# Performance work log

Hardware: AMD Instinct MI355X
Metric: run time of the kernel (lower is better)

The kernel has to match this reference:

```python
import math
import jax, jax.numpy as jnp
import numpy as np

HEADS = 8
DIM_HEAD = 64
NUM_MEM_KV = 16


def alibi_slopes(heads):
    def pow2_slopes(n):
        start = 2 ** (-(2 ** -(math.log2(n) - 3)))
        return [start * (start ** i) for i in range(n)]
    if math.log2(heads).is_integer():
        return np.asarray(pow2_slopes(heads), dtype=np.float32)
    cp2 = 2 ** math.floor(math.log2(heads))
    extra = pow2_slopes(2 * cp2)[0::2][: heads - cp2]
    return np.asarray(pow2_slopes(cp2) + extra, dtype=np.float32)


def setup_inputs() -> dict:
    key = jax.random.key(0)
    ks = jax.random.split(key, 12)
    b, n, dim = 2, 2048, 512
    h, dh, mem = HEADS, DIM_HEAD, NUM_MEM_KV
    s = 0.02  # weight init scale for numerical sanity
    return {
        "x": jax.random.normal(ks[0], (b, n, dim), jnp.float32),
        "Wq": jax.random.normal(ks[1], (dim, h * dh), jnp.float32) * s,
        "Wk": jax.random.normal(ks[2], (dim, h * dh), jnp.float32) * s,
        "Wv": jax.random.normal(ks[3], (dim, h * dh), jnp.float32) * s,
        "mem_k": jax.random.normal(ks[4], (h, mem, dh), jnp.float32),
        "mem_v": jax.random.normal(ks[5], (h, mem, dh), jnp.float32),
        "pre_proj": jax.random.normal(ks[6], (h, h), jnp.float32),
        "post_proj": jax.random.normal(ks[7], (h, h), jnp.float32),
        "head_scale_params": jnp.ones((1, h, 1, 1), jnp.float32),
        "Wout": jax.random.normal(ks[8], (h * dh, dim), jnp.float32) * s,
        "bout": jnp.zeros((dim,), jnp.float32),
    }


def reference(x, Wq, Wk, Wv, mem_k, mem_v, pre_proj, post_proj,
              head_scale_params, Wout, bout):
    b, n, dim = x.shape
    h, dh, mem = HEADS, DIM_HEAD, NUM_MEM_KV
    scale = dh ** -0.5

    def split_heads(t):  # [b,n,h*dh] -> [b,h,n,dh]
        return t.reshape(b, n, h, dh).transpose(0, 2, 1, 3)

    q = split_heads(x @ Wq)
    k = split_heads(x @ Wk)
    v = split_heads(x @ Wv)

    # prepend learned memory key/values: k,v -> [b,h,mem+n,dh]
    k = jnp.concatenate([jnp.broadcast_to(mem_k, (b, h, mem, dh)), k], axis=2)
    v = jnp.concatenate([jnp.broadcast_to(mem_v, (b, h, mem, dh)), v], axis=2)
    j = mem + n

    dots = jnp.einsum('bhid,bhjd->bhij', q, k) * scale
    # talking heads (pre-softmax)
    dots = jnp.einsum('bhij,hk->bkij', dots, pre_proj)
    # alibi relative positional bias: arange(j) * slope per head
    slopes = jnp.asarray(alibi_slopes(h))  # [h]
    dots = dots + jnp.arange(j, dtype=dots.dtype)[None, None, None, :] * slopes[None, :, None, None]
    # causal mask (mem columns always visible); mask where col-mem > row
    neg = -jnp.finfo(dots.dtype).max
    causal = (jnp.arange(j)[None, :] - mem) > jnp.arange(n)[:, None]  # [n,j]
    dots = jnp.where(causal[None, None], neg, dots)

    attn = jax.nn.softmax(dots, axis=-1)
    # talking heads (post-softmax)
    attn = jnp.einsum('bhij,hk->bkij', attn, post_proj)

    out = jnp.einsum('bhij,bhjd->bhid', attn, v)
    out = out * head_scale_params
    out = out.transpose(0, 2, 1, 3).reshape(b, n, h * dh)
    return out @ Wout + bout
```

## Files before the change

### kernel.cpp

```cpp
#include <hip/hip_runtime.h>
#include <math.h>

namespace {
constexpr int B = 2;
constexpr int N = 2048;
constexpr int DIM = 512;
constexpr int H = 8;
constexpr int MEM = 16;
constexpr int J = MEM + N;
constexpr int CHUNK = 256;
constexpr int CMAX = 9;
constexpr float S2 = 0.125f * 1.4426950408889634f;
constexpr size_t EPB = 17170432;
}

typedef __attribute__((ext_vector_type(8))) short short8;
typedef __attribute__((ext_vector_type(4))) float floatx4;
typedef __attribute__((ext_vector_type(4))) unsigned short ushortx4;
typedef __attribute__((ext_vector_type(8))) unsigned short ushortx8;

__device__ inline unsigned short f2bf(float f) {
    unsigned int u = __float_as_uint(f);
    u += 0x7fffu + ((u >> 16) & 1u);
    return (unsigned short)(u >> 16);
}
__device__ inline unsigned int pk2bf(float a, float b) {
    return ((__float_as_uint(a) + 0x8000u) >> 16) |
           ((__float_as_uint(b) + 0x8000u) & 0xffff0000u);
}

__global__ __launch_bounds__(256)
void wt_conv(const float* __restrict__ Wq, const float* __restrict__ Wk,
             const float* __restrict__ Wv, const float* __restrict__ Wo,
             unsigned short* __restrict__ tq, unsigned short* __restrict__ tk,
             unsigned short* __restrict__ tv, unsigned short* __restrict__ to_)
{
    const int z = blockIdx.z;
    const float* __restrict__ W = (z == 0) ? Wq : (z == 1) ? Wk : (z == 2) ? Wv : Wo;
    unsigned short* __restrict__ WT = (z == 0) ? tq : (z == 1) ? tk : (z == 2) ? tv : to_;
    const int k0 = blockIdx.x * 64, n0 = blockIdx.y * 64;

    __shared__ __align__(16) unsigned short tile[64][72];
    const int t = threadIdx.x;
    const int rrow = t >> 4, rcol = (t & 15) * 4;
#pragma unroll
    for (int rr = 0; rr < 4; ++rr) {
        const int row = rrow + rr * 16;
        const float4 v = *(const float4*)(W + (size_t)(k0 + row) * DIM + n0 + rcol);
        tile[rcol + 0][row] = f2bf(v.x);
        tile[rcol + 1][row] = f2bf(v.y);
        tile[rcol + 2][row] = f2bf(v.z);
        tile[rcol + 3][row] = f2bf(v.w);
    }
    __syncthreads();
    const int orow = t >> 2, oseg = (t & 3) * 16;
    *(ushortx8*)(WT + (size_t)(n0 + orow) * DIM + k0 + oseg) =
        *(const ushortx8*)(&tile[orow][oseg]);
    *(ushortx8*)(WT + (size_t)(n0 + orow) * DIM + k0 + oseg + 8) =
        *(const ushortx8*)(&tile[orow][oseg + 8]);
}

__global__ __launch_bounds__(256)
void qkv_gemm(const float* __restrict__ x, const unsigned short* __restrict__ tq,
              const unsigned short* __restrict__ tk, const unsigned short* __restrict__ tv,
              unsigned short* __restrict__ q16, unsigned short* __restrict__ k16,
              unsigned short* __restrict__ vt16)
{
    const int which = blockIdx.z;
    const unsigned short* __restrict__ WT = (which == 0) ? tq : (which == 1) ? tk : tv;
    const int t = threadIdx.x;
    const int lane = t & 63, w = t >> 6;
    const int iL = lane & 15, quad = lane >> 4;
    const int mb = blockIdx.x * 64;
    const int n0 = blockIdx.y * 64;

    __shared__ __align__(16) unsigned short As[2][64][32];
    __shared__ __align__(16) unsigned short Bs[2][64][32];

    const int ar0 = t >> 3, as4 = (t & 7) * 4;
    const int br0 = t >> 2, bs8 = (t & 3) * 8;

    floatx4 acc[4];
#pragma unroll
    for (int ng = 0; ng < 4; ++ng) acc[ng] = (floatx4){0.f, 0.f, 0.f, 0.f};

    {
        const float4 v0 = *(const float4*)(x + (size_t)(mb + ar0) * DIM + as4);
        const float4 v1 = *(const float4*)(x + (size_t)(mb + ar0 + 32) * DIM + as4);
        ushortx4 o0 = { f2bf(v0.x), f2bf(v0.y), f2bf(v0.z), f2bf(v0.w) };
        ushortx4 o1 = { f2bf(v1.x), f2bf(v1.y), f2bf(v1.z), f2bf(v1.w) };
        *(ushortx4*)(&As[0][ar0][as4]) = o0;
        *(ushortx4*)(&As[0][ar0 + 32][as4]) = o1;
        *(ushortx8*)(&Bs[0][br0][bs8]) =
            *(const ushortx8*)(WT + (size_t)(n0 + br0) * DIM + bs8);
    }
    __syncthreads();

#pragma unroll
    for (int it = 0; it < 16; ++it) {
        const int buf = it & 1;
        if (it + 1 < 16) {
            const int k0 = (it + 1) * 32;
            const float4 v0 = *(const float4*)(x + (size_t)(mb + ar0) * DIM + k0 + as4);
            const float4 v1 = *(const float4*)(x + (size_t)(mb + ar0 + 32) * DIM + k0 + as4);
            const ushortx8 bv =
                *(const ushortx8*)(WT + (size_t)(n0 + br0) * DIM + k0 + bs8);
            ushortx4 o0 = { f2bf(v0.x), f2bf(v0.y), f2bf(v0.z), f2bf(v0.w) };
            ushortx4 o1 = { f2bf(v1.x), f2bf(v1.y), f2bf(v1.z), f2bf(v1.w) };
            *(ushortx4*)(&As[buf ^ 1][ar0][as4]) = o0;
            *(ushortx4*)(&As[buf ^ 1][ar0 + 32][as4]) = o1;
            *(ushortx8*)(&Bs[buf ^ 1][br0][bs8]) = bv;
        }
        const short8 af = *(const short8*)(&As[buf][w * 16 + iL][quad * 8]);
#pragma unroll
        for (int ng = 0; ng < 4; ++ng) {
            const short8 bf = *(const short8*)(&Bs[buf][ng * 16 + iL][quad * 8]);
            acc[ng] = __builtin_amdgcn_mfma_f32_16x16x32_bf16(af, bf, acc[ng], 0, 0, 0);
        }
        __syncthreads();
    }

    const int mbw = mb + w * 16;
    const int h0 = n0 >> 6;
    if (which == 2) {
#pragma unroll
        for (int ng = 0; ng < 4; ++ng) {
            const int d = ng * 16 + iL;
#pragma unroll
            for (int r = 0; r < 4; ++r) {
                const int m = mbw + quad * 4 + r;
                const int bb = m >> 11, ii = m & (N - 1);
                vt16[((size_t)(bb * H + h0) * 64 + d) * J + MEM + ii] = f2bf(acc[ng][r]);
            }
        }
    } else {
        unsigned short* dst = (which == 0) ? q16 : k16;
#pragma unroll
        for (int ng = 0; ng < 4; ++ng) {
            const int d = ng * 16 + iL;
#pragma unroll
            for (int r = 0; r < 4; ++r) {
                const int m = mbw + quad * 4 + r;
                const int bb = m >> 11, ii = m & (N - 1);
                const size_t rowbase = (which == 0)
                    ? ((size_t)(bb * H + h0) * N + ii)
                    : ((size_t)(bb * H + h0) * J + MEM + ii);
                dst[rowbase * 64 + d] = f2bf(acc[ng][r]);
            }
        }
    }
}

__global__ void memkv_copy(const float* __restrict__ mem_k, const float* __restrict__ mem_v,
                           unsigned short* __restrict__ k16, unsigned short* __restrict__ vt16)
{
    const int idx = blockIdx.x * 256 + threadIdx.x;
    if (idx >= H * MEM * 64) return;
    const int h0 = idx >> 10;
    const int rd = idx & 1023;
    const int r = rd >> 6, d = rd & 63;
    const unsigned short kk = f2bf(mem_k[idx]);
    const unsigned short vv = f2bf(mem_v[idx]);
#pragma unroll
    for (int bb = 0; bb < B; ++bb) {
        k16[((size_t)(bb * H + h0) * J + r) * 64 + d] = kk;
        vt16[((size_t)(bb * H + h0) * 64 + d) * J + r] = vv;
    }
}

__global__ __launch_bounds__(256)
void attn_scores(const unsigned short* __restrict__ qb, const unsigned short* __restrict__ kb,
                 const float* __restrict__ prep, float* __restrict__ lbuf,
                 unsigned short* __restrict__ e16)
{
    const int c = blockIdx.x, tt = 127 - blockIdx.y, b = blockIdx.z;
    const int i0 = tt * 16;
    const int jlim = i0 + 32;
    const int jstart = c * CHUNK;
    if (jstart >= jlim) return;
    const int jend = min(jstart + CHUNK, jlim);

    __shared__ __align__(16) unsigned short q_s[8][16][64];
    __shared__ __align__(16) float pre_s[64];
    const int t = threadIdx.x;
    if (t < 64) pre_s[t] = prep[t];
#pragma unroll
    for (int u4 = 0; u4 < 4; ++u4) {
        const int u = t + u4 * 256;
        const int h = u >> 7, rem = u & 127, i = rem >> 3, seg = (rem & 7) * 8;
        *(ushortx8*)(&q_s[h][i][seg]) =
            *(const ushortx8*)(qb + ((size_t)(b * H + h) * N + i0 + i) * 64 + seg);
    }
    __syncthreads();

    const int lane = t & 63, w = t >> 6;
    const int iL = lane & 15, quad = lane >> 4;
    const int i = i0 + iL;
    const size_t ebase = (size_t)b * EPB + (size_t)(8 * tt * tt + 24 * tt) * 128;

    float l_acc[8];
#pragma unroll
    for (int h1 = 0; h1 < 8; ++h1) l_acc[h1] = 0.f;

    bool any = false;
    for (int j0 = jstart + w * 16; j0 < jend; j0 += 64) {
        any = true;
        float dots[8][4];
#pragma unroll
        for (int h1 = 0; h1 < 8; ++h1)
#pragma unroll
            for (int r = 0; r < 4; ++r) dots[h1][r] = 0.f;

        const unsigned short* kp0 = kb + ((size_t)(b * H) * J + j0 + iL) * 64 + quad * 8;
        short8 kc0 = *(const short8*)kp0;
        short8 kc1 = *(const short8*)(kp0 + 32);
#pragma unroll
        for (int h0 = 0; h0 < 8; ++h0) {
            short8 kn0, kn1;
            if (h0 < 7) {
                const unsigned short* kpn =
                    kb + ((size_t)(b * H + h0 + 1) * J + j0 + iL) * 64 + quad * 8;
                kn0 = *(const short8*)kpn;
                kn1 = *(const short8*)(kpn + 32);
            }
            const short8 qf0 = *(const short8*)(&q_s[h0][iL][quad * 8]);
            const short8 qf1 = *(const short8*)(&q_s[h0][iL][quad * 8 + 32]);
            floatx4 a = {0.f, 0.f, 0.f, 0.f};
            a = __builtin_amdgcn_mfma_f32_16x16x32_bf16(kc0, qf0, a, 0, 0, 0);
            a = __builtin_amdgcn_mfma_f32_16x16x32_bf16(kc1, qf1, a, 0, 0, 0);
            const float4 pr0 = *(const float4*)(&pre_s[h0 * 8]);
            const float4 pr1 = *(const float4*)(&pre_s[h0 * 8 + 4]);
#pragma unroll
            for (int r = 0; r < 4; ++r) {
                const float av = a[r];
                dots[0][r] = fmaf(av, pr0.x, dots[0][r]);
                dots[1][r] = fmaf(av, pr0.y, dots[1][r]);
                dots[2][r] = fmaf(av, pr0.z, dots[2][r]);
                dots[3][r] = fmaf(av, pr0.w, dots[3][r]);
                dots[4][r] = fmaf(av, pr1.x, dots[4][r]);
                dots[5][r] = fmaf(av, pr1.y, dots[5][r]);
                dots[6][r] = fmaf(av, pr1.z, dots[6][r]);
                dots[7][r] = fmaf(av, pr1.w, dots[7][r]);
            }
            kc0 = kn0; kc1 = kn1;
        }

        unsigned int epk[4][4];
        float etmp[4];
#pragma unroll
        for (int h1 = 0; h1 < 8; ++h1) {
            const float slopeE = 1.4426950408889634f / (float)(2 << h1);
#pragma unroll
            for (int r = 0; r < 4; ++r) {
                const int j = j0 + quad * 4 + r;
                const bool vis = (j - MEM) <= i;
                const float e = vis ? exp2f(fmaf(dots[h1][r], S2, slopeE * (float)(j - i - MEM)))
                                    : 0.f;
                l_acc[h1] += e;
                if (h1 & 1) epk[r][h1 >> 1] = pk2bf(etmp[r], e);
                else        etmp[r] = e;
            }
        }
#pragma unroll
        for (int r = 0; r < 4; ++r) {
            uint4 o = make_uint4(epk[r][0], epk[r][1], epk[r][2], epk[r][3]);
            *(uint4*)(e16 + ebase + (size_t)((j0 + quad * 4 + r) * 16 + iL) * 8) = o;
        }
    }

#pragma unroll
    for (int h1 = 0; h1 < 8; ++h1) {
        float v = l_acc[h1];
        v += __shfl_xor(v, 16);
        v += __shfl_xor(v, 32);
        if (quad == 0 && any)
            atomicAdd(lbuf + ((size_t)(b * 128 + tt) * 8 + h1) * 16 + iL, v);
    }
}

__global__ __launch_bounds__(256)
void attn_pv2(const unsigned short* __restrict__ e16, const unsigned short* __restrict__ vt,
              const float* __restrict__ postp, const float* __restrict__ hsp,
              const float* __restrict__ lbuf, float* __restrict__ ao)
{
    const int c = blockIdx.x, tt = 127 - blockIdx.y, b = blockIdx.z;
    const int i0 = tt * 16;
    const int jlim = i0 + 32;
    const int jstart = c * CHUNK;
    if (jstart >= jlim) return;
    const int jend = min(jstart + CHUNK, jlim);
    const int nw = (jend - jstart + 31) >> 5;

    __shared__ __align__(16) unsigned short p2s[2][8][16][40];
    __shared__ __align__(16) float post_s[64];

    const int t = threadIdx.x;
    if (t < 64) post_s[t] = postp[t] * hsp[t & 7];

    const int lane = t & 63, w = t >> 6;
    const int iL = lane & 15, quad = lane >> 4;
    const int dW = w * 16 + iL;
    const int i_p = t & 15;
    const int jj = t >> 4;
    const size_t ebase = (size_t)b * EPB + (size_t)(8 * tt * tt + 24 * tt) * 128;

    float linv[8];
#pragma unroll
    for (int h1 = 0; h1 < 8; ++h1)
        linv[h1] = 1.0f / lbuf[((size_t)(b * 128 + tt) * 8 + h1) * 16 + i_p];

    floatx4 y[8];
#pragma unroll
    for (int h2 = 0; h2 < 8; ++h2) y[h2] = (floatx4){0.f, 0.f, 0.f, 0.f};

    ushortx8 evc[2], evn[2];
    {
        const int j0c = jstart + jj * 2;
        const int ja = min(j0c, jend - 1), jb2 = min(j0c + 1, jend - 1);
        evc[0] = *(const ushortx8*)(e16 + ebase + (size_t)(ja * 16 + i_p) * 8);
        evc[1] = *(const ushortx8*)(e16 + ebase + (size_t)(jb2 * 16 + i_p) * 8);
    }
    __syncthreads();

    for (int n = 0; n < nw; ++n) {
        const int jw0 = jstart + n * 32;
        {
            const int j0n = jstart + (n + 1) * 32 + jj * 2;
            const int ja = min(j0n, jend - 1), jb2 = min(j0n + 1, jend - 1);
            evn[0] = *(const ushortx8*)(e16 + ebase + (size_t)(ja * 16 + i_p) * 8);
            evn[1] = *(const ushortx8*)(e16 + ebase + (size_t)(jb2 * 16 + i_p) * 8);
        }
        float p2[2][8];
#pragma unroll
        for (int s = 0; s < 2; ++s) {
#pragma unroll
            for (int h2 = 0; h2 < 8; ++h2) p2[s][h2] = 0.f;
            const int j = jw0 + jj * 2 + s;
            if (j < jend) {
#pragma unroll
                for (int h1 = 0; h1 < 8; ++h1) {
                    const float e = __uint_as_float((unsigned int)(unsigned short)evc[s][h1] << 16)
                                    * linv[h1];
                    const float4 po0 = *(const float4*)(&post_s[h1 * 8]);
                    const float4 po1 = *(const float4*)(&post_s[h1 * 8 + 4]);
                    p2[s][0] = fmaf(e, po0.x, p2[s][0]);
                    p2[s][1] = fmaf(e, po0.y, p2[s][1]);
                    p2[s][2] = fmaf(e, po0.z, p2[s][2]);
                    p2[s][3] = fmaf(e, po0.w, p2[s][3]);
                    p2[s][4] = fmaf(e, po1.x, p2[s][4]);
                    p2[s][5] = fmaf(e, po1.y, p2[s][5]);
                    p2[s][6] = fmaf(e, po1.z, p2[s][6]);
                    p2[s][7] = fmaf(e, po1.w, p2[s][7]);
                }
            }
        }
        const int buf = n & 1;
#pragma unroll
        for (int h2 = 0; h2 < 8; ++h2)
            *(unsigned int*)(&p2s[buf][h2][i_p][jj * 2]) = pk2bf(p2[0][h2], p2[1][h2]);
        __syncthreads();

        int jbv = jw0 + quad * 8;
        if (jbv > J - 8) jbv = J - 8;
#pragma unroll
        for (int h2 = 0; h2 < 8; ++h2) {
            const short8 aF = *(const short8*)(&p2s[buf][h2][iL][quad * 8]);
            const short8 bF = *(const short8*)(vt + ((size_t)(b * H + h2) * 64 + dW) * J + jbv);
            y[h2] = __builtin_amdgcn_mfma_f32_16x16x32_bf16(aF, bF, y[h2], 0, 0, 0);
        }
        evc[0] = evn[0]; evc[1] = evn[1];
    }

#pragma unroll
    for (int h2 = 0; h2 < 8; ++h2) {
#pragma unroll
        for (int r = 0; r < 4; ++r) {
            const int ii = i0 + quad * 4 + r;
            atomicAdd(ao + ((size_t)b * N + ii) * DIM + h2 * 64 + dW, y[h2][r]);
        }
    }
}

__global__ __launch_bounds__(256)
void out_gemm(const float* __restrict__ ain, const unsigned short* __restrict__ WT,
              const float* __restrict__ bo, float* __restrict__ out)
{
    const int t = threadIdx.x;
    const int lane = t & 63, w = t >> 6;
    const int iL = lane & 15, quad = lane >> 4;
    const int mb = blockIdx.x * 64;
    const int n0 = blockIdx.y * 64;

    __shared__ __align__(16) unsigned short As[2][64][32];
    __shared__ __align__(16) unsigned short Bs[2][64][32];

    const int ar0 = t >> 3, as4 = (t & 7) * 4;
    const int br0 = t >> 2, bs8 = (t & 3) * 8;

    floatx4 acc[4];
#pragma unroll
    for (int ng = 0; ng < 4; ++ng) acc[ng] = (floatx4){0.f, 0.f, 0.f, 0.f};

    {
        const float4 v0 = *(const float4*)(ain + (size_t)(mb + ar0) * DIM + as4);
        const float4 v1 = *(const float4*)(ain + (size_t)(mb + ar0 + 32) * DIM + as4);
        ushortx4 o0 = { f2bf(v0.x), f2bf(v0.y), f2bf(v0.z), f2bf(v0.w) };
        ushortx4 o1 = { f2bf(v1.x), f2bf(v1.y), f2bf(v1.z), f2bf(v1.w) };
        *(ushortx4*)(&As[0][ar0][as4]) = o0;
        *(ushortx4*)(&As[0][ar0 + 32][as4]) = o1;
        *(ushortx8*)(&Bs[0][br0][bs8]) =
            *(const ushortx8*)(WT + (size_t)(n0 + br0) * DIM + bs8);
    }
    __syncthreads();

#pragma unroll
    for (int it = 0; it < 16; ++it) {
        const int buf = it & 1;
        if (it + 1 < 16) {
            const int k0 = (it + 1) * 32;
            const float4 v0 = *(const float4*)(ain + (size_t)(mb + ar0) * DIM + k0 + as4);
            const float4 v1 = *(const float4*)(ain + (size_t)(mb + ar0 + 32) * DIM + k0 + as4);
            const ushortx8 bv =
                *(const ushortx8*)(WT + (size_t)(n0 + br0) * DIM + k0 + bs8);
            ushortx4 o0 = { f2bf(v0.x), f2bf(v0.y), f2bf(v0.z), f2bf(v0.w) };
            ushortx4 o1 = { f2bf(v1.x), f2bf(v1.y), f2bf(v1.z), f2bf(v1.w) };
            *(ushortx4*)(&As[buf ^ 1][ar0][as4]) = o0;
            *(ushortx4*)(&As[buf ^ 1][ar0 + 32][as4]) = o1;
            *(ushortx8*)(&Bs[buf ^ 1][br0][bs8]) = bv;
        }
        const short8 af = *(const short8*)(&As[buf][w * 16 + iL][quad * 8]);
#pragma unroll
        for (int ng = 0; ng < 4; ++ng) {
            const short8 bf = *(const short8*)(&Bs[buf][ng * 16 + iL][quad * 8]);
            acc[ng] = __builtin_amdgcn_mfma_f32_16x16x32_bf16(af, bf, acc[ng], 0, 0, 0);
        }
        __syncthreads();
    }

    const int mbw = mb + w * 16;
#pragma unroll
    for (int ng = 0; ng < 4; ++ng) {
        const int n = n0 + ng * 16 + iL;
        const float bias = bo[n];
#pragma unroll
        for (int r = 0; r < 4; ++r) {
            const int m = mbw + quad * 4 + r;
            out[(size_t)m * DIM + n] = acc[ng][r] + bias;
        }
    }
}

extern "C" void kernel_launch(void* const* d_in, const int* in_sizes, int n_in,
                              void* d_out, int out_size, void* d_ws, size_t ws_size,
                              hipStream_t stream)
{
    (void)in_sizes; (void)n_in; (void)out_size; (void)ws_size;
    const float* x      = (const float*)d_in[0];
    const float* Wq     = (const float*)d_in[1];
    const float* Wk     = (const float*)d_in[2];
    const float* Wv     = (const float*)d_in[3];
    const float* mem_k  = (const float*)d_in[4];
    const float* mem_v  = (const float*)d_in[5];
    const float* pre_p  = (const float*)d_in[6];
    const float* post_p = (const float*)d_in[7];
    const float* hs     = (const float*)d_in[8];
    const float* Wo     = (const float*)d_in[9];
    const float* bo     = (const float*)d_in[10];
    float* out = (float*)d_out;

    constexpr size_t NAO  = (size_t)B * N * DIM;
    constexpr size_t NLB  = (size_t)B * 128 * H * 16;
    constexpr size_t NW   = (size_t)DIM * DIM;
    constexpr size_t NQ   = (size_t)B * H * N * 64;
    constexpr size_t NK   = (size_t)B * H * J * 64;

    float* ws = (float*)d_ws;
    float* ao   = ws;
    float* lbuf = ao + NAO;
    unsigned short* wtq  = (unsigned short*)(lbuf + NLB);
    unsigned short* wtk  = wtq + NW;
    unsigned short* wtv  = wtk + NW;
    unsigned short* wto  = wtv + NW;
    unsigned short* q16  = wto + NW;
    unsigned short* k16  = q16 + NQ;
    unsigned short* v16  = k16 + NK;
    unsigned short* e16  = v16 + NK;

    wt_conv<<<dim3(8, 8, 4), 256, 0, stream>>>(Wq, Wk, Wv, Wo, wtq, wtk, wtv, wto);
    qkv_gemm<<<dim3(64, 8, 3), 256, 0, stream>>>(x, wtq, wtk, wtv, q16, k16, v16);
    memkv_copy<<<dim3(32), 256, 0, stream>>>(mem_k, mem_v, k16, v16);
    hipMemsetAsync(ao, 0, (NAO + NLB) * sizeof(float), stream);
    attn_scores<<<dim3(CMAX, 128, B), 256, 0, stream>>>(q16, k16, pre_p, lbuf, e16);
    attn_pv2<<<dim3(CMAX, 128, B), 256, 0, stream>>>(e16, v16, post_p, hs, lbuf, ao);
    out_gemm<<<dim3(64, 8), 256, 0, stream>>>(ao, wto, bo, out);
}
```

Baseline: 236.8 us.

## Preconvert x to bf16, swizzle q smem, deepen prefetch, packed FMAs, reorder grid

Adds a separate kernel that converts x to bf16 once, so qkv_gemm loads bf16 tiles directly instead of converting fp32 inside every tile load. attn_scores XOR-swizzles the q shared-memory layout to avoid bank conflicts and prefetches K two heads ahead. Both attention kernels switch to packed float2 multiply-adds. attn_pv2 prefetches the score tiles three windows ahead and hoists the V fragment loads before the barrier. The grid is reordered so the row-tile index is blockIdx.x and chunks run in reverse, which changes block scheduling order. The cost is an extra kernel launch, a bf16 copy of x in the workspace, and higher register pressure from the deeper prefetch.

Measured after the change: 244.3 us. +3.1%, slower.

```diff
diff --git a/kernel.cpp b/kernel.cpp
--- a/kernel.cpp
+++ b/kernel.cpp
@@ -9,12 +9,12 @@
 constexpr int MEM = 16;
 constexpr int J = MEM + N;
 constexpr int CHUNK = 256;
-constexpr int CMAX = 9;
 constexpr float S2 = 0.125f * 1.4426950408889634f;
 constexpr size_t EPB = 17170432;
 }
 
 typedef __attribute__((ext_vector_type(8))) short short8;
+typedef __attribute__((ext_vector_type(2))) float floatx2;
 typedef __attribute__((ext_vector_type(4))) float floatx4;
 typedef __attribute__((ext_vector_type(4))) unsigned short ushortx4;
 typedef __attribute__((ext_vector_type(8))) unsigned short ushortx8;
@@ -27,6 +27,17 @@
 __device__ inline unsigned int pk2bf(float a, float b) {
     return ((__float_as_uint(a) + 0x8000u) >> 16) |
            ((__float_as_uint(b) + 0x8000u) & 0xffff0000u);
+}
+
+__global__ __launch_bounds__(256)
+void x_conv(const float* __restrict__ x, unsigned short* __restrict__ x16)
+{
+    const size_t base = ((size_t)blockIdx.x * 256 + threadIdx.x) * 8;
+    const float4 a = *(const float4*)(x + base);
+    const float4 b = *(const float4*)(x + base + 4);
+    ushortx8 o = { f2bf(a.x), f2bf(a.y), f2bf(a.z), f2bf(a.w),
+                   f2bf(b.x), f2bf(b.y), f2bf(b.z), f2bf(b.w) };
+    *(ushortx8*)(x16 + base) = o;
 }
 
 __global__ __launch_bounds__(256)
@@ -61,7 +72,7 @@
 }
 
 __global__ __launch_bounds__(256)
-void qkv_gemm(const float* __restrict__ x, const unsigned short* __restrict__ tq,
+void qkv_gemm(const unsigned short* __restrict__ x16, const unsigned short* __restrict__ tq,
               const unsigned short* __restrict__ tk, const unsigned short* __restrict__ tv,
               unsigned short* __restrict__ q16, unsigned short* __restrict__ k16,
               unsigned short* __restrict__ vt16)
@@ -77,22 +88,17 @@
     __shared__ __align__(16) unsigned short As[2][64][32];
     __shared__ __align__(16) unsigned short Bs[2][64][32];
 
-    const int ar0 = t >> 3, as4 = (t & 7) * 4;
-    const int br0 = t >> 2, bs8 = (t & 3) * 8;
+    const int r0 = t >> 2, s8 = (t & 3) * 8;
 
     floatx4 acc[4];
 #pragma unroll
     for (int ng = 0; ng < 4; ++ng) acc[ng] = (floatx4){0.f, 0.f, 0.f, 0.f};
 
     {
-        const float4 v0 = *(const float4*)(x + (size_t)(mb + ar0) * DIM + as4);
-        const float4 v1 = *(const float4*)(x + (size_t)(mb + ar0 + 32) * DIM + as4);
-        ushortx4 o0 = { f2bf(v0.x), f2bf(v0.y), f2bf(v0.z), f2bf(v0.w) };
-        ushortx4 o1 = { f2bf(v1.x), f2bf(v1.y), f2bf(v1.z), f2bf(v1.w) };
-        *(ushortx4*)(&As[0][ar0][as4]) = o0;
-        *(ushortx4*)(&As[0][ar0 + 32][as4]) = o1;
-        *(ushortx8*)(&Bs[0][br0][bs8]) =
-            *(const ushortx8*)(WT + (size_t)(n0 + br0) * DIM + bs8);
+        *(ushortx8*)(&As[0][r0][s8]) =
+            *(const ushortx8*)(x16 + (size_t)(mb + r0) * DIM + s8);
+        *(ushortx8*)(&Bs[0][r0][s8]) =
+            *(const ushortx8*)(WT + (size_t)(n0 + r0) * DIM + s8);
     }
     __syncthreads();
 
@@ -101,15 +107,10 @@
         const int buf = it & 1;
         if (it + 1 < 16) {
             const int k0 = (it + 1) * 32;
-            const float4 v0 = *(const float4*)(x + (size_t)(mb + ar0) * DIM + k0 + as4);
-            const float4 v1 = *(const float4*)(x + (size_t)(mb + ar0 + 32) * DIM + k0 + as4);
-            const ushortx8 bv =
-                *(const ushortx8*)(WT + (size_t)(n0 + br0) * DIM + k0 + bs8);
-            ushortx4 o0 = { f2bf(v0.x), f2bf(v0.y), f2bf(v0.z), f2bf(v0.w) };
-            ushortx4 o1 = { f2bf(v1.x), f2bf(v1.y), f2bf(v1.z), f2bf(v1.w) };
-            *(ushortx4*)(&As[buf ^ 1][ar0][as4]) = o0;
-            *(ushortx4*)(&As[buf ^ 1][ar0 + 32][as4]) = o1;
-            *(ushortx8*)(&Bs[buf ^ 1][br0][bs8]) = bv;
+            const ushortx8 av = *(const ushortx8*)(x16 + (size_t)(mb + r0) * DIM + k0 + s8);
+            const ushortx8 bv = *(const ushortx8*)(WT + (size_t)(n0 + r0) * DIM + k0 + s8);
+            *(ushortx8*)(&As[buf ^ 1][r0][s8]) = av;
+            *(ushortx8*)(&Bs[buf ^ 1][r0][s8]) = bv;
         }
         const short8 af = *(const short8*)(&As[buf][w * 16 + iL][quad * 8]);
 #pragma unroll
@@ -173,7 +174,7 @@
                  const float* __restrict__ prep, float* __restrict__ lbuf,
                  unsigned short* __restrict__ e16)
 {
-    const int c = blockIdx.x, tt = 127 - blockIdx.y, b = blockIdx.z;
+    const int tt = blockIdx.x, c = 8 - blockIdx.y, b = blockIdx.z;
     const int i0 = tt * 16;
     const int jlim = i0 + 32;
     const int jstart = c * CHUNK;
@@ -181,14 +182,14 @@
     const int jend = min(jstart + CHUNK, jlim);
 
     __shared__ __align__(16) unsigned short q_s[8][16][64];
-    __shared__ __align__(16) float pre_s[64];
+    __shared__ float pre_s[64];
     const int t = threadIdx.x;
     if (t < 64) pre_s[t] = prep[t];
 #pragma unroll
     for (int u4 = 0; u4 < 4; ++u4) {
         const int u = t + u4 * 256;
         const int h = u >> 7, rem = u & 127, i = rem >> 3, seg = (rem & 7) * 8;
-        *(ushortx8*)(&q_s[h][i][seg]) =
+        *(ushortx8*)(&q_s[h][i][seg ^ ((i & 7) << 3)]) =
             *(const ushortx8*)(qb + ((size_t)(b * H + h) * N + i0 + i) * 64 + seg);
     }
     __syncthreads();
@@ -196,6 +197,7 @@
     const int lane = t & 63, w = t >> 6;
     const int iL = lane & 15, quad = lane >> 4;
     const int i = i0 + iL;
+    const int sw = (iL & 7) << 3;
     const size_t ebase = (size_t)b * EPB + (size_t)(8 * tt * tt + 24 * tt) * 128;
 
     float l_acc[8];
@@ -205,44 +207,44 @@
     bool any = false;
     for (int j0 = jstart + w * 16; j0 < jend; j0 += 64) {
         any = true;
-        float dots[8][4];
-#pragma unroll
-        for (int h1 = 0; h1 < 8; ++h1)
-#pragma unroll
-            for (int r = 0; r < 4; ++r) dots[h1][r] = 0.f;
-
-        const unsigned short* kp0 = kb + ((size_t)(b * H) * J + j0 + iL) * 64 + quad * 8;
-        short8 kc0 = *(const short8*)kp0;
-        short8 kc1 = *(const short8*)(kp0 + 32);
+        floatx2 d01[8], d23[8];
+#pragma unroll
+        for (int h1 = 0; h1 < 8; ++h1) {
+            d01[h1] = (floatx2){0.f, 0.f};
+            d23[h1] = (floatx2){0.f, 0.f};
+        }
+
+        const unsigned short* kbase = kb + ((size_t)(b * H) * J + j0 + iL) * 64 + quad * 8;
+        const size_t hstride = (size_t)J * 64;
+        short8 ka0 = *(const short8*)(kbase);
+        short8 ka1 = *(const short8*)(kbase + 32);
+        short8 kb0_ = *(const short8*)(kbase + hstride);
+        short8 kb1_ = *(const short8*)(kbase + hstride + 32);
 #pragma unroll
         for (int h0 = 0; h0 < 8; ++h0) {
-            short8 kn0, kn1;
-            if (h0 < 7) {
-                const unsigned short* kpn =
-                    kb + ((size_t)(b * H + h0 + 1) * J + j0 + iL) * 64 + quad * 8;
-                kn0 = *(const short8*)kpn;
-                kn1 = *(const short8*)(kpn + 32);
+            short8 kc0_, kc1_;
+            if (h0 < 6) {
+                const unsigned short* kpn = kbase + (size_t)(h0 + 2) * hstride;
+                kc0_ = *(const short8*)(kpn);
+                kc1_ = *(const short8*)(kpn + 32);
             }
-            const short8 qf0 = *(const short8*)(&q_s[h0][iL][quad * 8]);
-            const short8 qf1 = *(const short8*)(&q_s[h0][iL][quad * 8 + 32]);
+            const short8 qf0 = *(const short8*)(&q_s[h0][iL][(quad * 8) ^ sw]);
+            const short8 qf1 = *(const short8*)(&q_s[h0][iL][(quad * 8 + 32) ^ sw]);
             floatx4 a = {0.f, 0.f, 0.f, 0.f};
-            a = __builtin_amdgcn_mfma_f32_16x16x32_bf16(kc0, qf0, a, 0, 0, 0);
-            a = __builtin_amdgcn_mfma_f32_16x16x32_bf16(kc1, qf1, a, 0, 0, 0);
+            a = __builtin_amdgcn_mfma_f32_16x16x32_bf16(ka0, qf0, a, 0, 0, 0);
+            a = __builtin_amdgcn_mfma_f32_16x16x32_bf16(ka1, qf1, a, 0, 0, 0);
+            const floatx2 av01 = {a[0], a[1]}, av23 = {a[2], a[3]};
             const float4 pr0 = *(const float4*)(&pre_s[h0 * 8]);
             const float4 pr1 = *(const float4*)(&pre_s[h0 * 8 + 4]);
-#pragma unroll
-            for (int r = 0; r < 4; ++r) {
-                const float av = a[r];
-                dots[0][r] = fmaf(av, pr0.x, dots[0][r]);
-                dots[1][r] = fmaf(av, pr0.y, dots[1][r]);
-                dots[2][r] = fmaf(av, pr0.z, dots[2][r]);
-                dots[3][r] = fmaf(av, pr0.w, dots[3][r]);
-                dots[4][r] = fmaf(av, pr1.x, dots[4][r]);
-                dots[5][r] = fmaf(av, pr1.y, dots[5][r]);
-                dots[6][r] = fmaf(av, pr1.z, dots[6][r]);
-                dots[7][r] = fmaf(av, pr1.w, dots[7][r]);
-            }
-            kc0 = kn0; kc1 = kn1;
+            d01[0] += av01 * pr0.x;  d23[0] += av23 * pr0.x;
+            d01[1] += av01 * pr0.y;  d23[1] += av23 * pr0.y;
+            d01[2] += av01 * pr0.z;  d23[2] += av23 * pr0.z;
+            d01[3] += av01 * pr0.w;  d23[3] += av23 * pr0.w;
+            d01[4] += av01 * pr1.x;  d23[4] += av23 * pr1.x;
+            d01[5] += av01 * pr1.y;  d23[5] += av23 * pr1.y;
+            d01[6] += av01 * pr1.z;  d23[6] += av23 * pr1.z;
+            d01[7] += av01 * pr1.w;  d23[7] += av23 * pr1.w;
+            ka0 = kb0_; ka1 = kb1_; kb0_ = kc0_; kb1_ = kc1_;
         }
 
         unsigned int epk[4][4];
@@ -250,11 +252,14 @@
 #pragma unroll
         for (int h1 = 0; h1 < 8; ++h1) {
             const float slopeE = 1.4426950408889634f / (float)(2 << h1);
+            const float dd0 = d01[h1][0], dd1 = d01[h1][1];
+            const float dd2 = d23[h1][0], dd3 = d23[h1][1];
 #pragma unroll
             for (int r = 0; r < 4; ++r) {
+                const float dv = (r == 0) ? dd0 : (r == 1) ? dd1 : (r == 2) ? dd2 : dd3;
                 const int j = j0 + quad * 4 + r;
                 const bool vis = (j - MEM) <= i;
-                const float e = vis ? exp2f(fmaf(dots[h1][r], S2, slopeE * (float)(j - i - MEM)))
+                const float e = vis ? exp2f(fmaf(dv, S2, slopeE * (float)(j - i - MEM)))
                                     : 0.f;
                 l_acc[h1] += e;
                 if (h1 & 1) epk[r][h1 >> 1] = pk2bf(etmp[r], e);
@@ -283,7 +288,7 @@
               const float* __restrict__ postp, const float* __restrict__ hsp,
               const float* __restrict__ lbuf, float* __restrict__ ao)
 {
-    const int c = blockIdx.x, tt = 127 - blockIdx.y, b = blockIdx.z;
+    const int tt = blockIdx.x, c = 8 - blockIdx.y, b = blockIdx.z;
     const int i0 = tt * 16;
     const int jlim = i0 + 32;
     const int jstart = c * CHUNK;
@@ -303,6 +308,7 @@
     const int i_p = t & 15;
     const int jj = t >> 4;
     const size_t ebase = (size_t)b * EPB + (size_t)(8 * tt * tt + 24 * tt) * 128;
+    const unsigned short* __restrict__ ep = e16 + ebase + (size_t)i_p * 8;
 
     float linv[8];
 #pragma unroll
@@ -313,62 +319,74 @@
 #pragma unroll
     for (int h2 = 0; h2 < 8; ++h2) y[h2] = (floatx4){0.f, 0.f, 0.f, 0.f};
 
-    ushortx8 evc[2], evn[2];
+    ushortx8 evA[2], evB[2], evC[2];
     {
         const int j0c = jstart + jj * 2;
-        const int ja = min(j0c, jend - 1), jb2 = min(j0c + 1, jend - 1);
-        evc[0] = *(const ushortx8*)(e16 + ebase + (size_t)(ja * 16 + i_p) * 8);
-        evc[1] = *(const ushortx8*)(e16 + ebase + (size_t)(jb2 * 16 + i_p) * 8);
+        int ja = min(j0c, jend - 1), jb2 = min(j0c + 1, jend - 1);
+        evA[0] = *(const ushortx8*)(ep + (size_t)(ja * 16) * 8);
+        evA[1] = *(const ushortx8*)(ep + (size_t)(jb2 * 16) * 8);
+        ja = min(j0c + 32, jend - 1); jb2 = min(j0c + 33, jend - 1);
+        evB[0] = *(const ushortx8*)(ep + (size_t)(ja * 16) * 8);
+        evB[1] = *(const ushortx8*)(ep + (size_t)(jb2 * 16) * 8);
+        ja = min(j0c + 64, jend - 1); jb2 = min(j0c + 65, jend - 1);
+        evC[0] = *(const ushortx8*)(ep + (size_t)(ja * 16) * 8);
+        evC[1] = *(const ushortx8*)(ep + (size_t)(jb2 * 16) * 8);
     }
     __syncthreads();
 
     for (int n = 0; n < nw; ++n) {
         const int jw0 = jstart + n * 32;
+        const int buf = n & 1;
+
+        int jbv = jw0 + quad * 8;
+        if (jbv > J - 8) jbv = J - 8;
+        short8 bF[8];
+#pragma unroll
+        for (int h2 = 0; h2 < 8; ++h2)
+            bF[h2] = *(const short8*)(vt + ((size_t)(b * H + h2) * 64 + dW) * J + jbv);
+
+        ushortx8 evT0, evT1;
         {
-            const int j0n = jstart + (n + 1) * 32 + jj * 2;
+            const int wn = (n + 3 < nw) ? n + 3 : nw - 1;
+            const int j0n = jstart + wn * 32 + jj * 2;
             const int ja = min(j0n, jend - 1), jb2 = min(j0n + 1, jend - 1);
-            evn[0] = *(const ushortx8*)(e16 + ebase + (size_t)(ja * 16 + i_p) * 8);
-            evn[1] = *(const ushortx8*)(e16 + ebase + (size_t)(jb2 * 16 + i_p) * 8);
-        }
-        float p2[2][8];
+            evT0 = *(const ushortx8*)(ep + (size_t)(ja * 16) * 8);
+            evT1 = *(const ushortx8*)(ep + (size_t)(jb2 * 16) * 8);
+        }
+
+        floatx2 p2v[2][4];
 #pragma unroll
         for (int s = 0; s < 2; ++s) {
 #pragma unroll
-            for (int h2 = 0; h2 < 8; ++h2) p2[s][h2] = 0.f;
+            for (int q = 0; q < 4; ++q) p2v[s][q] = (floatx2){0.f, 0.f};
             const int j = jw0 + jj * 2 + s;
             if (j < jend) {
 #pragma unroll
                 for (int h1 = 0; h1 < 8; ++h1) {
-                    const float e = __uint_as_float((unsigned int)(unsigned short)evc[s][h1] << 16)
-                                    * linv[h1];
-                    const float4 po0 = *(const float4*)(&post_s[h1 * 8]);
-                    const float4 po1 = *(const float4*)(&post_s[h1 * 8 + 4]);
-                    p2[s][0] = fmaf(e, po0.x, p2[s][0]);
-                    p2[s][1] = fmaf(e, po0.y, p2[s][1]);
-                    p2[s][2] = fmaf(e, po0.z, p2[s][2]);
-                    p2[s][3] = fmaf(e, po0.w, p2[s][3]);
-                    p2[s][4] = fmaf(e, po1.x, p2[s][4]);
-                    p2[s][5] = fmaf(e, po1.y, p2[s][5]);
-                    p2[s][6] = fmaf(e, po1.z, p2[s][6]);
-                    p2[s][7] = fmaf(e, po1.w, p2[s][7]);
+                    const float e = __uint_as_float(
+                        (unsigned int)(unsigned short)evA[s][h1] << 16) * linv[h1];
+                    const floatx2* po = (const floatx2*)(&post_s[h1 * 8]);
+                    p2v[s][0] += e * po[0];
+                    p2v[s][1] += e * po[1];
+                    p2v[s][2] += e * po[2];
+                    p2v[s][3] += e * po[3];
                 }
             }
         }
-        const int buf = n & 1;
 #pragma unroll
         for (int h2 = 0; h2 < 8; ++h2)
-            *(unsigned int*)(&p2s[buf][h2][i_p][jj * 2]) = pk2bf(p2[0][h2], p2[1][h2]);
+            *(unsigned int*)(&p2s[buf][h2][i_p][jj * 2]) =
+                pk2bf(p2v[0][h2 >> 1][h2 & 1], p2v[1][h2 >> 1][h2 & 1]);
         __syncthreads();
 
-        int jbv = jw0 + quad * 8;
-        if (jbv > J - 8) jbv = J - 8;
 #pragma unroll
         for (int h2 = 0; h2 < 8; ++h2) {
             const short8 aF = *(const short8*)(&p2s[buf][h2][iL][quad * 8]);
-            const short8 bF = *(const short8*)(vt + ((size_t)(b * H + h2) * 64 + dW) * J + jbv);
-            y[h2] = __builtin_amdgcn_mfma_f32_16x16x32_bf16(aF, bF, y[h2], 0, 0, 0);
-        }
-        evc[0] = evn[0]; evc[1] = evn[1];
+            y[h2] = __builtin_amdgcn_mfma_f32_16x16x32_bf16(aF, bF[h2], y[h2], 0, 0, 0);
+        }
+        evA[0] = evB[0]; evA[1] = evB[1];
+        evB[0] = evC[0]; evB[1] = evC[1];
+        evC[0] = evT0;   evC[1] = evT1;
     }
 
 #pragma unroll
@@ -473,6 +491,7 @@
     constexpr size_t NW   = (size_t)DIM * DIM;
     constexpr size_t NQ   = (size_t)B * H * N * 64;
     constexpr size_t NK   = (size_t)B * H * J * 64;
+    constexpr size_t NX   = (size_t)B * N * DIM;
 
     float* ws = (float*)d_ws;
     float* ao   = ws;
@@ -484,13 +503,15 @@
     unsigned short* q16  = wto + NW;
     unsigned short* k16  = q16 + NQ;
     unsigned short* v16  = k16 + NK;
-    unsigned short* e16  = v16 + NK;
-
+    unsigned short* x16  = v16 + NK;
+    unsigned short* e16  = x16 + NX;
+
+    x_conv<<<dim3(1024), 256, 0, stream>>>(x, x16);
     wt_conv<<<dim3(8, 8, 4), 256, 0, stream>>>(Wq, Wk, Wv, Wo, wtq, wtk, wtv, wto);
-    qkv_gemm<<<dim3(64, 8, 3), 256, 0, stream>>>(x, wtq, wtk, wtv, q16, k16, v16);
+    qkv_gemm<<<dim3(64, 8, 3), 256, 0, stream>>>(x16, wtq, wtk, wtv, q16, k16, v16);
     memkv_copy<<<dim3(32), 256, 0, stream>>>(mem_k, mem_v, k16, v16);
     hipMemsetAsync(ao, 0, (NAO + NLB) * sizeof(float), stream);
-    attn_scores<<<dim3(CMAX, 128, B), 256, 0, stream>>>(q16, k16, pre_p, lbuf, e16);
-    attn_pv2<<<dim3(CMAX, 128, B), 256, 0, stream>>>(e16, v16, post_p, hs, lbuf, ao);
+    attn_scores<<<dim3(128, 9, B), 256, 0, stream>>>(q16, k16, pre_p, lbuf, e16);
+    attn_pv2<<<dim3(128, 9, B), 256, 0, stream>>>(e16, v16, post_p, hs, lbuf, ao);
     out_gemm<<<dim3(64, 8), 256, 0, stream>>>(ao, wto, bo, out);
 }
```
